# Kernel tuning notes

Measured on AMD Instinct MI355X. Metric: run time of the kernel, lower is better.

The kernel has to match this reference:

```python
import jax, jax.numpy as jnp
import numpy as np

DA = 256      # aux input feature dim
DENSE = 512   # SLAM dense units


def setup_inputs() -> dict:
    key = jax.random.key(0)
    k1, k2, k3, k4 = jax.random.split(key, 4)
    x_main = jax.random.normal(k1, (1, 128, 512, 256), dtype=jnp.float32)  # [1,T,M,K]
    x_aux = jax.random.normal(k2, (256, 128, DA), dtype=jnp.float32)       # [K,T,Da]
    W = jax.random.normal(k3, (DA, DENSE), dtype=jnp.float32) / np.sqrt(DA)
    b = jax.random.normal(k4, (DENSE,), dtype=jnp.float32) * 0.01
    return {"x_main": x_main, "x_aux": x_aux, "W": W, "b": b}


def reference(x_main, x_aux, W, b):
    # SLAM aux dense (+relu), applied to every aux slice at once: [K,T,Da] -> [K,T,dense]
    aux_out = jax.nn.relu(jnp.einsum("ktd,de->kte", x_aux, W) + b)
    main = jnp.squeeze(x_main, axis=0)  # [T,M,K]
    # per-slice matmul main[t] @ aux_out[:,t,:] batched over T
    stacked = jnp.einsum("tmk,kte->tme", main, aux_out)  # [T,M,dense]
    # expand_dims(-1) then expand_dims(0)
    return stacked[None, :, :, :, None]  # [1,T,M,dense,1]
```

## Files before the change

kernel.cpp:

```cpp
#include <hip/hip_runtime.h>


typedef __attribute__((ext_vector_type(8))) short  bf16x8;
typedef __attribute__((ext_vector_type(4))) float  f32x4;
typedef __attribute__((ext_vector_type(4))) unsigned int uint4v;

#define T_DIM 128
#define M_DIM 512
#define K_DIM 256
#define DA    256
#define DENSE 512
#define AUX_T_STRIDE (K_DIM * DENSE)
#define CHUNK_G_STRIDE (DENSE * 8)

__device__ __forceinline__ unsigned short f2bf(float f) {
    unsigned u = __builtin_bit_cast(unsigned, f);
    unsigned r = (u + 0x7fffu + ((u >> 16) & 1u)) >> 16;
    return (unsigned short)r;
}
__device__ __forceinline__ unsigned pack2(float lo, float hi) {
    return (unsigned)f2bf(lo) | ((unsigned)f2bf(hi) << 16);
}

__global__ __launch_bounds__(256) void wchunk_kernel(const float* __restrict__ W,
                                                     unsigned short* __restrict__ Wc) {
    int c = blockIdx.x * 256 + threadIdx.x;
    int g = c >> 9;
    int e = c & 511;
    float f[8];
#pragma unroll
    for (int j = 0; j < 8; ++j) f[j] = W[(g * 8 + j) * DENSE + e];
    uint4v w;
    w.x = pack2(f[0], f[1]); w.y = pack2(f[2], f[3]);
    w.z = pack2(f[4], f[5]); w.w = pack2(f[6], f[7]);
    *reinterpret_cast<uint4v*>(Wc + (size_t)c * 8) = w;
}

__global__ __launch_bounds__(256) void aux_kernel(const float* __restrict__ xaux,
                                                  const unsigned short* __restrict__ Wc,
                                                  const float* __restrict__ bias,
                                                  unsigned short* __restrict__ auxc) {
    const int eb = blockIdx.x * 128;
    const int rb = blockIdx.y;
    const int t  = rb >> 1;
    const int kb = (rb & 1) * 128;
    const int lane = threadIdx.x & 63, wid = threadIdx.x >> 6;
    const int wk = (wid & 1) * 64;
    const int we = (wid >> 1) * 64;
    const int l15 = lane & 15, lg = lane >> 4;

    f32x4 acc[4][4];
#pragma unroll
    for (int i = 0; i < 4; ++i)
#pragma unroll
        for (int j = 0; j < 4; ++j) acc[i][j] = (f32x4)0.0f;

#pragma unroll
    for (int ds = 0; ds < DA / 32; ++ds) {
        bf16x8 wf[4];
#pragma unroll
        for (int j = 0; j < 4; ++j) {
            int e = eb + we + j * 16 + l15;
            wf[j] = *reinterpret_cast<const bf16x8*>(Wc + (size_t)(ds * 4 + lg) * CHUNK_G_STRIDE + (size_t)e * 8);
        }
        bf16x8 xf[4];
#pragma unroll
        for (int i = 0; i < 4; ++i) {
            int k = kb + wk + i * 16 + l15;
            const float* p = xaux + ((size_t)k * T_DIM + t) * DA + ds * 32 + lg * 8;
            f32x4 f0 = *reinterpret_cast<const f32x4*>(p);
            f32x4 f1 = *reinterpret_cast<const f32x4*>(p + 4);
            uint4v w;
            w.x = pack2(f0.x, f0.y); w.y = pack2(f0.z, f0.w);
            w.z = pack2(f1.x, f1.y); w.w = pack2(f1.z, f1.w);
            xf[i] = __builtin_bit_cast(bf16x8, w);
        }
#pragma unroll
        for (int i = 0; i < 4; ++i)
#pragma unroll
            for (int j = 0; j < 4; ++j)
                acc[i][j] = __builtin_amdgcn_mfma_f32_16x16x32_bf16(xf[i], wf[j], acc[i][j], 0, 0, 0);
    }

#pragma unroll
    for (int i = 0; i < 4; ++i) {
        int k0 = kb + wk + i * 16 + lg * 4;
#pragma unroll
        for (int j = 0; j < 4; ++j) {
            int e = eb + we + j * 16 + l15;
            float bv = bias[e];
            float v0 = fmaxf(acc[i][j].x + bv, 0.0f);
            float v1 = fmaxf(acc[i][j].y + bv, 0.0f);
            float v2 = fmaxf(acc[i][j].z + bv, 0.0f);
            float v3 = fmaxf(acc[i][j].w + bv, 0.0f);
            uint2 o; o.x = pack2(v0, v1); o.y = pack2(v2, v3);
            size_t idx = (size_t)t * AUX_T_STRIDE + (size_t)(k0 >> 3) * CHUNK_G_STRIDE
                       + (size_t)e * 8 + (k0 & 7);
            *reinterpret_cast<uint2*>(auxc + idx) = o;
        }
    }
}

__global__ __launch_bounds__(256) void main_kernel(const float* __restrict__ xmain,
                                                   const unsigned short* __restrict__ auxc,
                                                   float* __restrict__ out) {
    const int eb = blockIdx.x * 128;
    const int mb = blockIdx.y * 128;
    const int t  = blockIdx.z;
    const int lane = threadIdx.x & 63, wid = threadIdx.x >> 6;
    const int wm = (wid & 1) * 64;
    const int we = (wid >> 1) * 64;
    const int l15 = lane & 15, lg = lane >> 4;

    const float* At = xmain + (size_t)t * M_DIM * K_DIM;
    const unsigned short* Bt = auxc + (size_t)t * AUX_T_STRIDE;

    f32x4 acc[4][4];
#pragma unroll
    for (int i = 0; i < 4; ++i)
#pragma unroll
        for (int j = 0; j < 4; ++j) acc[i][j] = (f32x4)0.0f;

#pragma unroll
    for (int ks = 0; ks < K_DIM / 32; ++ks) {
        bf16x8 af[4];
#pragma unroll
        for (int i = 0; i < 4; ++i) {
            int e = eb + we + i * 16 + l15;
            af[i] = *reinterpret_cast<const bf16x8*>(Bt + (size_t)(ks * 4 + lg) * CHUNK_G_STRIDE + (size_t)e * 8);
        }
        bf16x8 mf[4];
#pragma unroll
        for (int j = 0; j < 4; ++j) {
            int m = mb + wm + j * 16 + l15;
            const float* p = At + (size_t)m * K_DIM + ks * 32 + lg * 8;
            f32x4 f0 = *reinterpret_cast<const f32x4*>(p);
            f32x4 f1 = *reinterpret_cast<const f32x4*>(p + 4);
            uint4v w;
            w.x = pack2(f0.x, f0.y); w.y = pack2(f0.z, f0.w);
            w.z = pack2(f1.x, f1.y); w.w = pack2(f1.z, f1.w);
            mf[j] = __builtin_bit_cast(bf16x8, w);
        }
#pragma unroll
        for (int i = 0; i < 4; ++i)
#pragma unroll
            for (int j = 0; j < 4; ++j)
                acc[i][j] = __builtin_amdgcn_mfma_f32_16x16x32_bf16(af[i], mf[j], acc[i][j], 0, 0, 0);
    }

#pragma unroll
    for (int i = 0; i < 4; ++i) {
        int e0 = eb + we + i * 16 + lg * 4;
#pragma unroll
        for (int j = 0; j < 4; ++j) {
            int m = mb + wm + j * 16 + l15;
            *reinterpret_cast<f32x4*>(out + (size_t)t * M_DIM * DENSE + (size_t)m * DENSE + e0) = acc[i][j];
        }
    }
}

extern "C" void kernel_launch(void* const* d_in, const int* in_sizes, int n_in,
                              void* d_out, int out_size, void* d_ws, size_t ws_size,
                              hipStream_t stream) {
    const float* x_main = (const float*)d_in[0];
    const float* x_aux  = (const float*)d_in[1];
    const float* W      = (const float*)d_in[2];
    const float* b      = (const float*)d_in[3];
    float* out = (float*)d_out;

    unsigned short* Wc   = (unsigned short*)d_ws;
    unsigned short* auxc = (unsigned short*)((char*)d_ws + (1 << 19));

    wchunk_kernel<<<64, 256, 0, stream>>>(W, Wc);
    aux_kernel<<<dim3(4, 256), 256, 0, stream>>>(x_aux, Wc, b, auxc);
    main_kernel<<<dim3(4, 4, 128), 256, 0, stream>>>(x_main, auxc, out);
}
```

Baseline: 316.9 us.

## Stage aux rows in LDS, double-buffer operand loads, swizzle main block order

The aux kernel now uses 512-thread blocks that stage a 128x256 slice of x_aux into shared memory as bf16 once. Each block covers all 512 dense columns, so the per-e-tile re-reads and re-conversions of x_aux go away, and W fragments are double-buffered in registers. The main kernel software-pipelines its global loads (A/B register double buffering) to overlap load latency with MFMA. It also uses a 1D grid with a swizzle that spreads consecutive blocks across different t slices, presumably to balance across XCDs. The cost is higher register pressure, with 32 accumulators plus two W buffers in aux, which may reduce occupancy.

```diff
diff --git a/kernel.cpp b/kernel.cpp
--- a/kernel.cpp
+++ b/kernel.cpp
@@ -4,6 +4,7 @@
 typedef __attribute__((ext_vector_type(8))) short  bf16x8;
 typedef __attribute__((ext_vector_type(4))) float  f32x4;
 typedef __attribute__((ext_vector_type(4))) unsigned int uint4v;
+typedef __attribute__((ext_vector_type(2))) unsigned int uint2v;
 
 #define T_DIM 128
 #define M_DIM 512
@@ -36,58 +37,75 @@
     *reinterpret_cast<uint4v*>(Wc + (size_t)c * 8) = w;
 }
 
-__global__ __launch_bounds__(256) void aux_kernel(const float* __restrict__ xaux,
+__global__ __launch_bounds__(512) void aux_kernel(const float* __restrict__ xaux,
                                                   const unsigned short* __restrict__ Wc,
                                                   const float* __restrict__ bias,
                                                   unsigned short* __restrict__ auxc) {
-    const int eb = blockIdx.x * 128;
-    const int rb = blockIdx.y;
-    const int t  = rb >> 1;
-    const int kb = (rb & 1) * 128;
-    const int lane = threadIdx.x & 63, wid = threadIdx.x >> 6;
+    __shared__ unsigned short xa[128][264];
+    const int kb = blockIdx.x * 128;
+    const int t  = blockIdx.y;
+    const int tid = threadIdx.x;
+    const int lane = tid & 63, wid = tid >> 6;
+
+    {
+        const int d0 = (tid & 63) * 4;
+        const int kr = tid >> 6;
+#pragma unroll
+        for (int p = 0; p < 16; ++p) {
+            int k = p * 8 + kr;
+            const float* src = xaux + ((size_t)(kb + k) * T_DIM + t) * DA + d0;
+            f32x4 v = *reinterpret_cast<const f32x4*>(src);
+            uint2v o; o.x = pack2(v.x, v.y); o.y = pack2(v.z, v.w);
+            *reinterpret_cast<uint2v*>(&xa[k][d0]) = o;
+        }
+    }
+    __syncthreads();
+
     const int wk = (wid & 1) * 64;
-    const int we = (wid >> 1) * 64;
+    const int we = (wid >> 1) * 128;
     const int l15 = lane & 15, lg = lane >> 4;
 
-    f32x4 acc[4][4];
+    f32x4 acc[4][8];
 #pragma unroll
     for (int i = 0; i < 4; ++i)
 #pragma unroll
-        for (int j = 0; j < 4; ++j) acc[i][j] = (f32x4)0.0f;
-
-#pragma unroll
-    for (int ds = 0; ds < DA / 32; ++ds) {
-        bf16x8 wf[4];
-#pragma unroll
-        for (int j = 0; j < 4; ++j) {
-            int e = eb + we + j * 16 + l15;
-            wf[j] = *reinterpret_cast<const bf16x8*>(Wc + (size_t)(ds * 4 + lg) * CHUNK_G_STRIDE + (size_t)e * 8);
-        }
-        bf16x8 xf[4];
-#pragma unroll
-        for (int i = 0; i < 4; ++i) {
-            int k = kb + wk + i * 16 + l15;
-            const float* p = xaux + ((size_t)k * T_DIM + t) * DA + ds * 32 + lg * 8;
-            f32x4 f0 = *reinterpret_cast<const f32x4*>(p);
-            f32x4 f1 = *reinterpret_cast<const f32x4*>(p + 4);
-            uint4v w;
-            w.x = pack2(f0.x, f0.y); w.y = pack2(f0.z, f0.w);
-            w.z = pack2(f1.x, f1.y); w.w = pack2(f1.z, f1.w);
-            xf[i] = __builtin_bit_cast(bf16x8, w);
-        }
-#pragma unroll
-        for (int i = 0; i < 4; ++i)
-#pragma unroll
-            for (int j = 0; j < 4; ++j)
-                acc[i][j] = __builtin_amdgcn_mfma_f32_16x16x32_bf16(xf[i], wf[j], acc[i][j], 0, 0, 0);
+        for (int j = 0; j < 8; ++j) acc[i][j] = (f32x4)0.0f;
+
+#define AUX_LOAD_WF(dst, dsv)                                                              \
+    do {                                                                                   \
+        _Pragma("unroll") for (int j = 0; j < 8; ++j) {                                    \
+            int e = we + j * 16 + l15;                                                     \
+            dst[j] = *reinterpret_cast<const bf16x8*>(                                     \
+                Wc + (size_t)((dsv) * 4 + lg) * CHUNK_G_STRIDE + (size_t)e * 8);           \
+        }                                                                                  \
+    } while (0)
+
+#define AUX_COMPUTE(wfc, dsv)                                                              \
+    do {                                                                                   \
+        bf16x8 xf[4];                                                                      \
+        _Pragma("unroll") for (int i = 0; i < 4; ++i)                                      \
+            xf[i] = *reinterpret_cast<const bf16x8*>(&xa[wk + i * 16 + l15][(dsv) * 32 + lg * 8]); \
+        _Pragma("unroll") for (int i = 0; i < 4; ++i)                                      \
+            _Pragma("unroll") for (int j = 0; j < 8; ++j)                                  \
+                acc[i][j] = __builtin_amdgcn_mfma_f32_16x16x32_bf16(xf[i], wfc[j], acc[i][j], 0, 0, 0); \
+    } while (0)
+
+    bf16x8 wfA[8], wfB[8];
+    AUX_LOAD_WF(wfA, 0);
+#pragma unroll
+    for (int ds = 0; ds < 8; ds += 2) {
+        AUX_LOAD_WF(wfB, ds + 1);
+        AUX_COMPUTE(wfA, ds);
+        if (ds + 2 < 8) { AUX_LOAD_WF(wfA, ds + 2); }
+        AUX_COMPUTE(wfB, ds + 1);
     }
 
 #pragma unroll
     for (int i = 0; i < 4; ++i) {
         int k0 = kb + wk + i * 16 + lg * 4;
 #pragma unroll
-        for (int j = 0; j < 4; ++j) {
-            int e = eb + we + j * 16 + l15;
+        for (int j = 0; j < 8; ++j) {
+            int e = we + j * 16 + l15;
             float bv = bias[e];
             float v0 = fmaxf(acc[i][j].x + bv, 0.0f);
             float v1 = fmaxf(acc[i][j].y + bv, 0.0f);
@@ -99,14 +117,19 @@
             *reinterpret_cast<uint2*>(auxc + idx) = o;
         }
     }
+#undef AUX_LOAD_WF
+#undef AUX_COMPUTE
 }
 
 __global__ __launch_bounds__(256) void main_kernel(const float* __restrict__ xmain,
                                                    const unsigned short* __restrict__ auxc,
                                                    float* __restrict__ out) {
-    const int eb = blockIdx.x * 128;
-    const int mb = blockIdx.y * 128;
-    const int t  = blockIdx.z;
+    const int bid = blockIdx.x;
+    const int swz = ((bid & 7) << 8) | (bid >> 3);
+    const int t   = swz >> 4;
+    const int r4  = swz & 15;
+    const int eb  = (r4 & 3) * 128;
+    const int mb  = (r4 >> 2) * 128;
     const int lane = threadIdx.x & 63, wid = threadIdx.x >> 6;
     const int wm = (wid & 1) * 64;
     const int we = (wid >> 1) * 64;
@@ -121,32 +144,46 @@
 #pragma unroll
         for (int j = 0; j < 4; ++j) acc[i][j] = (f32x4)0.0f;
 
-#pragma unroll
-    for (int ks = 0; ks < K_DIM / 32; ++ks) {
-        bf16x8 af[4];
-#pragma unroll
-        for (int i = 0; i < 4; ++i) {
-            int e = eb + we + i * 16 + l15;
-            af[i] = *reinterpret_cast<const bf16x8*>(Bt + (size_t)(ks * 4 + lg) * CHUNK_G_STRIDE + (size_t)e * 8);
-        }
-        bf16x8 mf[4];
-#pragma unroll
-        for (int j = 0; j < 4; ++j) {
-            int m = mb + wm + j * 16 + l15;
-            const float* p = At + (size_t)m * K_DIM + ks * 32 + lg * 8;
-            f32x4 f0 = *reinterpret_cast<const f32x4*>(p);
-            f32x4 f1 = *reinterpret_cast<const f32x4*>(p + 4);
-            uint4v w;
-            w.x = pack2(f0.x, f0.y); w.y = pack2(f0.z, f0.w);
-            w.z = pack2(f1.x, f1.y); w.w = pack2(f1.z, f1.w);
-            mf[j] = __builtin_bit_cast(bf16x8, w);
-        }
-#pragma unroll
-        for (int i = 0; i < 4; ++i)
-#pragma unroll
-            for (int j = 0; j < 4; ++j)
-                acc[i][j] = __builtin_amdgcn_mfma_f32_16x16x32_bf16(af[i], mf[j], acc[i][j], 0, 0, 0);
-    }
+#define MAIN_LOAD(afd, m0d, m1d, ksv)                                                      \
+    do {                                                                                   \
+        _Pragma("unroll") for (int i = 0; i < 4; ++i)                                      \
+            afd[i] = *reinterpret_cast<const bf16x8*>(                                     \
+                Bt + (size_t)((ksv) * 4 + lg) * CHUNK_G_STRIDE                             \
+                   + (size_t)(eb + we + i * 16 + l15) * 8);                                \
+        _Pragma("unroll") for (int j = 0; j < 4; ++j) {                                    \
+            const float* p = At + (size_t)(mb + wm + j * 16 + l15) * K_DIM                 \
+                           + (ksv) * 32 + lg * 8;                                          \
+            m0d[j] = *reinterpret_cast<const f32x4*>(p);                                   \
+            m1d[j] = *reinterpret_cast<const f32x4*>(p + 4);                               \
+        }                                                                                  \
+    } while (0)
+
+#define MAIN_COMPUTE(afd, m0d, m1d)                                                        \
+    do {                                                                                   \
+        bf16x8 mf[4];                                                                      \
+        _Pragma("unroll") for (int j = 0; j < 4; ++j) {                                    \
+            uint4v w;                                                                      \
+            w.x = pack2(m0d[j].x, m0d[j].y); w.y = pack2(m0d[j].z, m0d[j].w);              \
+            w.z = pack2(m1d[j].x, m1d[j].y); w.w = pack2(m1d[j].z, m1d[j].w);              \
+            mf[j] = __builtin_bit_cast(bf16x8, w);                                         \
+        }                                                                                  \
+        _Pragma("unroll") for (int i = 0; i < 4; ++i)                                      \
+            _Pragma("unroll") for (int j = 0; j < 4; ++j)                                  \
+                acc[i][j] = __builtin_amdgcn_mfma_f32_16x16x32_bf16(afd[i], mf[j], acc[i][j], 0, 0, 0); \
+    } while (0)
+
+    bf16x8 afA[4], afB[4];
+    f32x4 m0A[4], m1A[4], m0B[4], m1B[4];
+    MAIN_LOAD(afA, m0A, m1A, 0);
+#pragma unroll
+    for (int ks = 0; ks < 8; ks += 2) {
+        MAIN_LOAD(afB, m0B, m1B, ks + 1);
+        MAIN_COMPUTE(afA, m0A, m1A);
+        if (ks + 2 < 8) { MAIN_LOAD(afA, m0A, m1A, ks + 2); }
+        MAIN_COMPUTE(afB, m0B, m1B);
+    }
+#undef MAIN_LOAD
+#undef MAIN_COMPUTE
 
 #pragma unroll
     for (int i = 0; i < 4; ++i) {
@@ -172,6 +209,6 @@
     unsigned short* auxc = (unsigned short*)((char*)d_ws + (1 << 19));
 
     wchunk_kernel<<<64, 256, 0, stream>>>(W, Wc);
-    aux_kernel<<<dim3(4, 256), 256, 0, stream>>>(x_aux, Wc, b, auxc);
-    main_kernel<<<dim3(4, 4, 128), 256, 0, stream>>>(x_main, auxc, out);
-}
+    aux_kernel<<<dim3(2, 128), 512, 0, stream>>>(x_aux, Wc, b, auxc);
+    main_kernel<<<2048, 256, 0, stream>>>(x_main, auxc, out);
+}
```

New measurement: 300.2 us. 5.3% less time.
